# Performance work log

Hardware: AMD Instinct MI355X
Metric: run time of the kernel (lower is better)

## Reference

```python
import jax, jax.numpy as jnp
import numpy as np

B, NUM_SLOTS, D, TOP_K = 2048, 128, 1024, 8
DH = D // 2  # route_mlp hidden


def setup_inputs() -> dict:
    key = jax.random.key(0)
    ks = jax.random.split(key, 16)
    s = 0.02
    return {
        "x": jax.random.normal(ks[0], (B, D), jnp.float32),
        "S": jax.random.normal(ks[1], (B, NUM_SLOTS, D), jnp.float32),
        # route_mlp: Linear(2D, D//2) -> GELU -> Linear(D//2, NUM_SLOTS)
        "w1": jax.random.normal(ks[2], (DH, 2 * D), jnp.float32) * s,
        "b1": jnp.zeros((DH,), jnp.float32),
        "w2": jax.random.normal(ks[3], (NUM_SLOTS, DH), jnp.float32) * s,
        "b2": jnp.zeros((NUM_SLOTS,), jnp.float32),
        # GRUCell(D, D): torch layout, gates ordered (r, z, n)
        "gru_wih": jax.random.normal(ks[4], (3 * D, D), jnp.float32) * s,
        "gru_whh": jax.random.normal(ks[5], (3 * D, D), jnp.float32) * s,
        "gru_bih": jnp.zeros((3 * D,), jnp.float32),
        "gru_bhh": jnp.zeros((3 * D,), jnp.float32),
        "wval": jax.random.normal(ks[6], (D, D), jnp.float32) * s,
        "bval": jnp.zeros((D,), jnp.float32),
        "wout": jax.random.normal(ks[7], (D, D), jnp.float32) * s,
        "bout": jnp.zeros((D,), jnp.float32),
        "tau": jnp.ones((1,), jnp.float32),
    }


def reference(x, S, w1, b1, w2, b2, gru_wih, gru_whh, gru_bih, gru_bhh,
              wval, bval, wout, bout, tau):
    # Routing: context = [x, mean over slots]
    slot_mean = S.mean(axis=1)                                  # [B, D]
    ctx = jnp.concatenate([x, slot_mean], axis=-1)              # [B, 2D]
    h = jax.nn.gelu(ctx @ w1.T + b1, approximate=False)         # [B, DH]
    route_logits = (h @ w2.T + b2) / (jnp.abs(tau) + 0.1)       # [B, NUM_SLOTS]

    topk_vals, topk_idx = jax.lax.top_k(route_logits, TOP_K)    # [B, K]
    topk_w = jax.nn.softmax(topk_vals, axis=-1)                 # [B, K]

    # Gather selected slot states
    slot_states = jnp.take_along_axis(S, topk_idx[:, :, None], axis=1)  # [B, K, D]

    # GRUCell (torch semantics). Input part shared across the K slots.
    gi = x @ gru_wih.T + gru_bih                                # [B, 3D]
    gh = slot_states @ gru_whh.T + gru_bhh                      # [B, K, 3D]
    gi_r, gi_z, gi_n = jnp.split(gi, 3, axis=-1)
    gh_r, gh_z, gh_n = jnp.split(gh, 3, axis=-1)
    r = jax.nn.sigmoid(gi_r[:, None, :] + gh_r)
    z = jax.nn.sigmoid(gi_z[:, None, :] + gh_z)
    n = jnp.tanh(gi_n[:, None, :] + r * gh_n)
    updated = (1.0 - z) * n + z * slot_states                   # [B, K, D]

    # Scatter updated states back into slot memory
    S_new = S.at[jnp.arange(B)[:, None], topk_idx].set(updated)

    # Weighted value readout
    values = updated @ wval.T + bval                            # [B, K, D]
    mixed = jnp.einsum('bkd,bk->bd', values, topk_w)            # [B, D]
    output = mixed @ wout.T + bout                              # [B, D]
    return output, S_new
```

## Files before the change

### kernel.cpp

```cpp
#include <hip/hip_runtime.h>
#include <math.h>
#include <stdint.h>

#define B_   2048
#define NS_  128
#define D_   1024
#define K_   8
#define DH_  512
#define G3_  3072

typedef unsigned short u16;
typedef short bf16x8 __attribute__((ext_vector_type(8)));
typedef float f32x4 __attribute__((ext_vector_type(4)));

__device__ __forceinline__ float bf2f(u16 u) {
  union { unsigned i; float f; } v; v.i = ((unsigned)u) << 16; return v.f;
}
__device__ __forceinline__ u16 f2bf(float f) {
  unsigned x = __float_as_uint(f);
  return (u16)((x + 0x7fffu + ((x >> 16) & 1u)) >> 16);
}

#define AS1C(p) ((const __attribute__((address_space(1))) void*)(uintptr_t)(p))
#define AS3(p)  ((__attribute__((address_space(3))) void*)(unsigned)(uintptr_t)(p))

template<int DO_COPY>
__global__ __launch_bounds__(256)
void sp_copymean(const float* __restrict__ S, float* __restrict__ Snew,
                 float* __restrict__ mean) {
  const int b = blockIdx.x;
  const int t = threadIdx.x, d0 = t * 4;
  const f32x4* src = (const f32x4*)(S + (size_t)b * NS_ * D_) + t;
  f32x4* dst = (f32x4*)(Snew + (size_t)b * NS_ * D_) + t;
  double a0 = 0, a1 = 0, a2 = 0, a3 = 0;
  #pragma unroll 4
  for (int s = 0; s < NS_; ++s) {
    f32x4 v = __builtin_nontemporal_load(src);
    if (DO_COPY) __builtin_nontemporal_store(v, dst);
    a0 += v[0]; a1 += v[1]; a2 += v[2]; a3 += v[3];
    src += 256; dst += 256;
  }
  float4 m;
  m.x = (float)(a0 * (1.0 / 128.0)); m.y = (float)(a1 * (1.0 / 128.0));
  m.z = (float)(a2 * (1.0 / 128.0)); m.w = (float)(a3 * (1.0 / 128.0));
  *(float4*)&mean[(size_t)b * D_ + d0] = m;
}

__global__ __launch_bounds__(256)
void sp_prep(const float* __restrict__ x, const float* __restrict__ wih,
             const float* __restrict__ whh, const float* __restrict__ wout,
             const float* __restrict__ wval, const float* __restrict__ bval,
             const float* __restrict__ bout,
             u16* __restrict__ xb, u16* __restrict__ wihb,
             u16* __restrict__ whhb, u16* __restrict__ woutb,
             u16* __restrict__ wvalT, float* __restrict__ brow) {
  __shared__ u16 tile[64][65];
  const int blk = blockIdx.x;
  const int t = threadIdx.x;
  if (blk < 1024) {
    for (int i = blk * 256 + t; i < 2359296; i += 1024 * 256) {
      const float* s; u16* d; int off;
      if (i < 524288)       { s = x;    d = xb;    off = i; }
      else if (i < 1310720) { s = wih;  d = wihb;  off = i - 524288; }
      else if (i < 2097152) { s = whh;  d = whhb;  off = i - 1310720; }
      else                  { s = wout; d = woutb; off = i - 2097152; }
      float4 v = ((const float4*)s)[off];
      ushort4 o;
      o.x = f2bf(v.x); o.y = f2bf(v.y); o.z = f2bf(v.z); o.w = f2bf(v.w);
      ((ushort4*)d)[off] = o;
    }
  } else if (blk < 1280) {
    const int tb = blk - 1024;
    const int bx = tb & 15, by = tb >> 4;
    const int r = t >> 4, c4 = (t & 15) * 4;
    #pragma unroll
    for (int p = 0; p < 4; ++p) {
      const int row = by * 64 + p * 16 + r;
      float4 v = *(const float4*)&wval[(size_t)row * D_ + bx * 64 + c4];
      tile[p * 16 + r][c4 + 0] = f2bf(v.x);
      tile[p * 16 + r][c4 + 1] = f2bf(v.y);
      tile[p * 16 + r][c4 + 2] = f2bf(v.z);
      tile[p * 16 + r][c4 + 3] = f2bf(v.w);
    }
    __syncthreads();
    #pragma unroll
    for (int p = 0; p < 4; ++p) {
      const int jr = p * 16 + r;
      ushort4 o;
      o.x = tile[c4 + 0][jr];
      o.y = tile[c4 + 1][jr];
      o.z = tile[c4 + 2][jr];
      o.w = tile[c4 + 3][jr];
      *(ushort4*)&wvalT[(size_t)(bx * 64 + jr) * D_ + by * 64 + c4] = o;
    }
  } else {
    const int w = t >> 6, l = t & 63;
    const int i = (blk - 1280) * 4 + w;
    float s = 0.f;
    const float* wr = &wout[(size_t)i * D_ + l * 16];
    const float* bv = &bval[l * 16];
    #pragma unroll
    for (int j = 0; j < 16; j += 4) {
      float4 w4 = *(const float4*)&wr[j];
      float4 b4 = *(const float4*)&bv[j];
      s += w4.x * b4.x + w4.y * b4.y + w4.z * b4.z + w4.w * b4.w;
    }
    #pragma unroll
    for (int off = 32; off > 0; off >>= 1) s += __shfl_xor(s, off);
    if (l == 0) brow[i] = s + bout[i];
  }
}

__global__ __launch_bounds__(256)
void sp_gemm1(const float* __restrict__ x, const float* __restrict__ mean,
              const float* __restrict__ w1, const float* __restrict__ bias1,
              float* __restrict__ h) {
  __shared__ float As[16][68];
  __shared__ float Bs[16][36];
  int wg = blockIdx.x;
  wg = (wg & 7) * 64 + (wg >> 3);
  const int n0 = (wg & 15) * 32;
  const int m0 = (wg >> 4) * 64;
  const int t = threadIdx.x;
  const int tx = t & 15, ty = t >> 4;
  float acc[4][2] = {};
  const int sr = t >> 2, sc = (t & 3) * 4;
  for (int k0 = 0; k0 < 2 * D_; k0 += 16) {
    const float* src = (k0 < D_) ? (x + k0) : (mean + (k0 - D_));
    float4 va = *(const float4*)&src[(size_t)(m0 + sr) * D_ + sc];
    As[sc + 0][sr] = va.x; As[sc + 1][sr] = va.y; As[sc + 2][sr] = va.z; As[sc + 3][sr] = va.w;
    if (t < 128) {
      const int bn = t >> 2, bc = (t & 3) * 4;
      float4 vb = *(const float4*)&w1[(size_t)(n0 + bn) * (2 * D_) + k0 + bc];
      Bs[bc + 0][bn] = vb.x; Bs[bc + 1][bn] = vb.y; Bs[bc + 2][bn] = vb.z; Bs[bc + 3][bn] = vb.w;
    }
    __syncthreads();
    #pragma unroll
    for (int kk = 0; kk < 16; ++kk) {
      float4 a = *(const float4*)&As[kk][ty * 4];
      float2 bb = *(const float2*)&Bs[kk][tx * 2];
      acc[0][0] = fmaf(a.x, bb.x, acc[0][0]); acc[0][1] = fmaf(a.x, bb.y, acc[0][1]);
      acc[1][0] = fmaf(a.y, bb.x, acc[1][0]); acc[1][1] = fmaf(a.y, bb.y, acc[1][1]);
      acc[2][0] = fmaf(a.z, bb.x, acc[2][0]); acc[2][1] = fmaf(a.z, bb.y, acc[2][1]);
      acc[3][0] = fmaf(a.w, bb.x, acc[3][0]); acc[3][1] = fmaf(a.w, bb.y, acc[3][1]);
    }
    __syncthreads();
  }
  #pragma unroll
  for (int i = 0; i < 4; ++i) {
    #pragma unroll
    for (int j = 0; j < 2; ++j) {
      const int r = m0 + ty * 4 + i, c = n0 + tx * 2 + j;
      float v = acc[i][j] + bias1[c];
      v = 0.5f * v * (1.0f + erff(v * 0.70710678118654752f));
      h[(size_t)r * DH_ + c] = v;
    }
  }
}

__global__ __launch_bounds__(64)
void sp_route_topk(const float* __restrict__ h, const float* __restrict__ w2,
                   const float* __restrict__ b2, const float* __restrict__ tau,
                   const float* __restrict__ S,
                   int* __restrict__ tki, float* __restrict__ tkw,
                   u16* __restrict__ slotb) {
  __shared__ float hs[DH_];
  __shared__ int sTki[K_];
  const int b = blockIdx.x, l = threadIdx.x;
  *(float4*)&hs[l * 4] = *(const float4*)&h[(size_t)b * DH_ + l * 4];
  *(float4*)&hs[256 + l * 4] = *(const float4*)&h[(size_t)b * DH_ + 256 + l * 4];
  __syncthreads();
  const double invd = 1.0 / ((double)fabsf(tau[0]) + 0.1);
  float v[2]; int id[2];
  #pragma unroll
  for (int c = 0; c < 2; ++c) {
    const int n = c * 64 + l;
    const float* wr = &w2[(size_t)n * DH_];
    double s = 0.0;
    for (int j = 0; j < DH_; j += 4) {
      float4 w4 = *(const float4*)&wr[j];
      s += (double)hs[j] * (double)w4.x;
      s += (double)hs[j + 1] * (double)w4.y;
      s += (double)hs[j + 2] * (double)w4.z;
      s += (double)hs[j + 3] * (double)w4.w;
    }
    v[c] = (float)((s + (double)b2[n]) * invd);
    id[c] = n;
  }
  float m0f = 0.f, sum = 0.f, mye = 0.f; int myi = 0;
  for (int r = 0; r < 8; ++r) {
    float mv; int mi;
    if (v[1] > v[0]) { mv = v[1]; mi = id[1]; } else { mv = v[0]; mi = id[0]; }
    #pragma unroll
    for (int off = 32; off > 0; off >>= 1) {
      float ov = __shfl_xor(mv, off);
      int oi = __shfl_xor(mi, off);
      if (ov > mv || (ov == mv && oi < mi)) { mv = ov; mi = oi; }
    }
    if (r == 0) m0f = mv;
    float er = expf(mv - m0f);
    sum += er;
    if (l == r) { mye = er; myi = mi; }
    if (mi == id[0]) v[0] = -3.0e38f;
    if (mi == id[1]) v[1] = -3.0e38f;
  }
  if (l < 8) {
    tki[b * K_ + l] = myi; tkw[b * K_ + l] = mye / sum;
    sTki[l] = myi;
  }
  __syncthreads();
  #pragma unroll
  for (int k = 0; k < K_; ++k) {
    const int s = sTki[k];
    const float4* src = (const float4*)&S[((size_t)b * NS_ + s) * D_];
    ushort4* dst = (ushort4*)&slotb[((size_t)b * K_ + k) * D_];
    #pragma unroll
    for (int c = 0; c < 4; ++c) {
      float4 vv = src[c * 64 + l];
      ushort4 o;
      o.x = f2bf(vv.x); o.y = f2bf(vv.y); o.z = f2bf(vv.z); o.w = f2bf(vv.w);
      dst[c * 64 + l] = o;
    }
  }
}

template<int EPI>
__global__ __launch_bounds__(256)
void sp_gemm_bf16(const u16* __restrict__ A, const u16* __restrict__ Bm,
                  void* __restrict__ Cv, const float* __restrict__ bias,
                  int M, int N, int Kd, int nbx) {
  __shared__ u16 lA[128 * 32];
  __shared__ u16 lB[128 * 32];
  int wg = blockIdx.x;
  {
    const int nwg = nbx * ((M + 127) >> 7);
    const int cpx = nwg >> 3;
    wg = (wg & 7) * cpx + (wg >> 3);
  }
  const int m0 = (wg / nbx) * 128, n0 = (wg % nbx) * 128;
  const int t = threadIdx.x;
  const int lane = t & 63;
  const int w = t >> 6;
  const int wm = w >> 1, wn = w & 1;

  f32x4 acc[4][4] = {};

  const int srow = t >> 2;
  const int scol = (t & 3) * 8;
  const u16* gA0 = A + (size_t)(m0 + srow) * Kd + scol;
  const u16* gA1 = A + (size_t)(m0 + 64 + srow) * Kd + scol;
  const u16* gB0 = Bm + (size_t)(n0 + srow) * Kd + scol;
  const u16* gB1 = Bm + (size_t)(n0 + 64 + srow) * Kd + scol;
  u16* lAw = &lA[(t & 192) * 8];
  u16* lBw = &lB[(t & 192) * 8];

  const int kb = (lane >> 4) * 8;
  const int rA = wm * 64 + (lane & 15);
  const int rB = wn * 64 + (lane & 15);

  for (int k0 = 0; k0 < Kd; k0 += 32) {
    __builtin_amdgcn_global_load_lds(AS1C(gA0 + k0), AS3(lAw), 16, 0, 0);
    __builtin_amdgcn_global_load_lds(AS1C(gA1 + k0), AS3(lAw + 2048), 16, 0, 0);
    __builtin_amdgcn_global_load_lds(AS1C(gB0 + k0), AS3(lBw), 16, 0, 0);
    __builtin_amdgcn_global_load_lds(AS1C(gB1 + k0), AS3(lBw + 2048), 16, 0, 0);
    __syncthreads();
    bf16x8 af[4], bfr[4];
    #pragma unroll
    for (int fm = 0; fm < 4; ++fm)
      af[fm] = *(const bf16x8*)&lA[(rA + fm * 16) * 32 + kb];
    #pragma unroll
    for (int fn = 0; fn < 4; ++fn)
      bfr[fn] = *(const bf16x8*)&lB[(rB + fn * 16) * 32 + kb];
    #pragma unroll
    for (int fm = 0; fm < 4; ++fm) {
      #pragma unroll
      for (int fn = 0; fn < 4; ++fn)
        acc[fm][fn] = __builtin_amdgcn_mfma_f32_16x16x32_bf16(af[fm], bfr[fn], acc[fm][fn], 0, 0, 0);
    }
    __syncthreads();
  }

  #pragma unroll
  for (int fm = 0; fm < 4; ++fm) {
    #pragma unroll
    for (int fn = 0; fn < 4; ++fn) {
      #pragma unroll
      for (int i = 0; i < 4; ++i) {
        const int r = m0 + wm * 64 + fm * 16 + (lane >> 4) * 4 + i;
        const int c = n0 + wn * 64 + fn * 16 + (lane & 15);
        float v = acc[fm][fn][i];
        if constexpr (EPI >= 2) v += bias[c];
        if constexpr (EPI == 0 || EPI == 2)
          ((float*)Cv)[(size_t)r * N + c] = v;
        else
          ((u16*)Cv)[(size_t)r * N + c] = f2bf(v);
      }
    }
  }
}

template<bool DIRECT>
__global__ __launch_bounds__(256, 2)
void sp_gh_gru(const u16* __restrict__ slotb, const u16* __restrict__ whhb,
               const u16* __restrict__ gib, const float* __restrict__ bih,
               const float* __restrict__ bhh, const int* __restrict__ tki,
               const float* __restrict__ tkw, float* __restrict__ dst,
               u16* __restrict__ umixb) {
  __shared__ u16 lA[128 * 32];
  __shared__ u16 lB[192 * 32];
  __shared__ int   sTki[128];
  __shared__ float sTkw[128];
  int wg = blockIdx.x;
  wg = (wg & 7) * 256 + (wg >> 3);
  const int mt = wg >> 4, db = wg & 15;
  const int m0 = mt * 128, d0 = db * 64;
  const int t = threadIdx.x;
  const int lane = t & 63, w = t >> 6;
  const int wm = w >> 1, wn = w & 1;
  const int lane15 = lane & 15, hi = lane >> 4;

  if (t < 128) { sTki[t] = tki[m0 + t]; sTkw[t] = tkw[m0 + t]; }

  f32x4 acc[4][6] = {};

  const int srow = t >> 2;
  const int scol = (t & 3) * 8;
  const u16* gA0 = slotb + (size_t)(m0 + srow) * D_ + scol;
  const u16* gA1 = slotb + (size_t)(m0 + 64 + srow) * D_ + scol;
  const u16* gB0 = whhb + (size_t)(d0 + srow) * D_ + scol;
  const u16* gB1 = whhb + (size_t)(D_ + d0 + srow) * D_ + scol;
  const u16* gB2 = whhb + (size_t)(2 * D_ + d0 + srow) * D_ + scol;
  u16* lAw = &lA[(t & 192) * 8];
  u16* lBw = &lB[(t & 192) * 8];

  const int kb = hi * 8;
  const int rA = wm * 64 + lane15;
  const int rB = wn * 32 + lane15;

  for (int k0 = 0; k0 < D_; k0 += 32) {
    __builtin_amdgcn_global_load_lds(AS1C(gA0 + k0), AS3(lAw), 16, 0, 0);
    __builtin_amdgcn_global_load_lds(AS1C(gA1 + k0), AS3(lAw + 2048), 16, 0, 0);
    __builtin_amdgcn_global_load_lds(AS1C(gB0 + k0), AS3(lBw), 16, 0, 0);
    __builtin_amdgcn_global_load_lds(AS1C(gB1 + k0), AS3(lBw + 2048), 16, 0, 0);
    __builtin_amdgcn_global_load_lds(AS1C(gB2 + k0), AS3(lBw + 4096), 16, 0, 0);
    __syncthreads();
    bf16x8 af[4], bfr[6];
    #pragma unroll
    for (int fm = 0; fm < 4; ++fm)
      af[fm] = *(const bf16x8*)&lA[(rA + fm * 16) * 32 + kb];
    #pragma unroll
    for (int g = 0; g < 3; ++g) {
      #pragma unroll
      for (int f = 0; f < 2; ++f)
        bfr[g * 2 + f] = *(const bf16x8*)&lB[(g * 64 + rB + f * 16) * 32 + kb];
    }
    #pragma unroll
    for (int fm = 0; fm < 4; ++fm) {
      #pragma unroll
      for (int fn = 0; fn < 6; ++fn)
        acc[fm][fn] = __builtin_amdgcn_mfma_f32_16x16x32_bf16(af[fm], bfr[fn], acc[fm][fn], 0, 0, 0);
    }
    __syncthreads();
  }

  #pragma unroll
  for (int fm = 0; fm < 4; ++fm) {
    const int rbase = wm * 64 + fm * 16 + hi * 4;
    const int bglob = (m0 + rbase) >> 3;
    #pragma unroll
    for (int f = 0; f < 2; ++f) {
      const int dg = d0 + wn * 32 + f * 16 + lane15;
      const float Gr = bf2f(gib[(size_t)bglob * G3_ + dg])          + bih[dg];
      const float Gz = bf2f(gib[(size_t)bglob * G3_ + D_ + dg])     + bih[D_ + dg];
      const float Gn = bf2f(gib[(size_t)bglob * G3_ + 2 * D_ + dg]) + bih[2 * D_ + dg];
      const float Br = bhh[dg], Bz = bhh[D_ + dg], Bn = bhh[2 * D_ + dg];
      float part = 0.f;
      #pragma unroll
      for (int i = 0; i < 4; ++i) {
        const int row = rbase + i;
        const int grow = m0 + row;
        const float slot = bf2f(slotb[(size_t)grow * D_ + dg]);
        const float rr = acc[fm][f][i] + Br;
        const float zz = acc[fm][f + 2][i] + Bz;
        const float nn = acc[fm][f + 4][i] + Bn;
        const float rg = 1.f / (1.f + expf(-(Gr + rr)));
        const float zg = 1.f / (1.f + expf(-(Gz + zz)));
        const float ng = tanhf(Gn + rg * nn);
        const float uv = (1.f - zg) * ng + zg * slot;
        part = fmaf(sTkw[row], uv, part);
        if (DIRECT)
          dst[((size_t)bglob * NS_ + sTki[row]) * D_ + dg] = uv;
        else
          dst[(size_t)grow * D_ + dg] = uv;
      }
      part += __shfl_xor(part, 16);
      if ((hi & 1) == 0)
        umixb[(size_t)bglob * D_ + dg] = f2bf(part);
    }
  }
}

__global__ __launch_bounds__(256)
void sp_copy_scatter(const float* __restrict__ S, const float* __restrict__ upd,
                     const int* __restrict__ tki, float* __restrict__ Snew) {
  const int b = blockIdx.x, t = threadIdx.x;
  const int d0 = t * 4;
  int idx[K_];
  #pragma unroll
  for (int k = 0; k < K_; ++k) idx[k] = tki[b * K_ + k];
  for (int s = 0; s < NS_; ++s) {
    int sk = -1;
    #pragma unroll
    for (int k = 0; k < K_; ++k) if (idx[k] == s) sk = k;
    float4 v;
    if (sk >= 0) v = *(const float4*)&upd[((size_t)b * K_ + sk) * D_ + d0];
    else         v = *(const float4*)&S[((size_t)b * NS_ + s) * D_ + d0];
    *(float4*)&Snew[((size_t)b * NS_ + s) * D_ + d0] = v;
  }
}

extern "C" void kernel_launch(void* const* d_in, const int* in_sizes, int n_in,
                              void* d_out, int out_size, void* d_ws, size_t ws_size,
                              hipStream_t stream) {
  const float* x    = (const float*)d_in[0];
  const float* S    = (const float*)d_in[1];
  const float* w1   = (const float*)d_in[2];
  const float* b1   = (const float*)d_in[3];
  const float* w2   = (const float*)d_in[4];
  const float* b2   = (const float*)d_in[5];
  const float* wih  = (const float*)d_in[6];
  const float* whh  = (const float*)d_in[7];
  const float* bih  = (const float*)d_in[8];
  const float* bhh  = (const float*)d_in[9];
  const float* wval = (const float*)d_in[10];
  const float* bval = (const float*)d_in[11];
  const float* wout = (const float*)d_in[12];
  const float* bout = (const float*)d_in[13];
  const float* tau  = (const float*)d_in[14];

  float* out  = (float*)d_out;
  float* Snew = out + (size_t)B_ * D_;

  const bool bigws = ws_size >= (size_t)400 * 1024 * 1024;
  char* bigbase = bigws ? (char*)d_ws : (char*)Snew;
  size_t bo = 0;
  auto balloc = [&](size_t bytes) -> void* {
    void* p = bigbase + bo; bo += (bytes + 255) & ~(size_t)255; return p;
  };

  float* mean  = (float*)balloc((size_t)B_ * D_ * 4);
  float* h     = (float*)balloc((size_t)B_ * DH_ * 4);
  u16* xb      = (u16*)balloc((size_t)B_ * D_ * 2);
  u16* wihb    = (u16*)balloc((size_t)G3_ * D_ * 2);
  u16* whhb    = (u16*)balloc((size_t)G3_ * D_ * 2);
  u16* woutb   = (u16*)balloc((size_t)D_ * D_ * 2);
  u16* wvalTb  = (u16*)balloc((size_t)D_ * D_ * 2);
  u16* Wrob    = (u16*)balloc((size_t)D_ * D_ * 2);
  u16* gib     = (u16*)balloc((size_t)B_ * G3_ * 2);
  u16* slotb   = (u16*)balloc((size_t)B_ * K_ * D_ * 2);
  u16* umixb   = (u16*)balloc((size_t)B_ * D_ * 2);
  float* brow  = (float*)balloc((size_t)D_ * 4);

  char* wsb = (char*)d_ws;
  size_t so = bigws ? bo : 0;
  auto salloc = [&](size_t bytes) -> void* {
    void* p = wsb + so; so += (bytes + 255) & ~(size_t)255; return p;
  };
  int*   tki = (int*)salloc((size_t)B_ * K_ * 4);
  float* tkw = (float*)salloc((size_t)B_ * K_ * 4);
  float* upd = bigws ? nullptr : (float*)salloc((size_t)B_ * K_ * D_ * 4);

  if (bigws) sp_copymean<1><<<B_, 256, 0, stream>>>(S, Snew, mean);
  else       sp_copymean<0><<<B_, 256, 0, stream>>>(S, Snew, mean);

  sp_prep<<<1536, 256, 0, stream>>>(x, wih, whh, wout, wval, bval, bout,
                                    xb, wihb, whhb, woutb, wvalTb, brow);

  sp_gemm_bf16<1><<<64, 256, 0, stream>>>(woutb, wvalTb, Wrob, nullptr, D_, D_, D_, 8);

  sp_gemm1<<<512, 256, 0, stream>>>(x, mean, w1, b1, h);

  sp_route_topk<<<B_, 64, 0, stream>>>(h, w2, b2, tau, S, tki, tkw, slotb);

  sp_gemm_bf16<1><<<384, 256, 0, stream>>>(xb, wihb, gib, nullptr, B_, G3_, D_, G3_ / 128);

  if (bigws)
    sp_gh_gru<true><<<2048, 256, 0, stream>>>(slotb, whhb, gib, bih, bhh,
                                              tki, tkw, Snew, umixb);
  else
    sp_gh_gru<false><<<2048, 256, 0, stream>>>(slotb, whhb, gib, bih, bhh,
                                               tki, tkw, upd, umixb);

  sp_gemm_bf16<2><<<128, 256, 0, stream>>>(umixb, Wrob, out, brow, B_, D_, D_, 8);

  if (!bigws)
    sp_copy_scatter<<<B_, 256, 0, stream>>>(S, upd, tki, Snew);
}
```

Before: 827.3 us.

## Merge copy/mean with weight prep and fuse independent GEMMs into one launch

The S copy/mean kernel and the weight-conversion prep kernel become one launch with block-range dispatch. The x@Wih GEMM, the routing GEMM1 (retiled to 64x64 per block) and the Wout·WvalT GEMM also become one launch, so independent work runs side by side. The gi GEMM moves ahead of top-k routing. This removes launch gaps and tail underutilisation, but larger LDS per block in the merged kernel may lower occupancy for the fp32 GEMM path.

```diff
diff --git a/kernel.cpp b/kernel.cpp
--- a/kernel.cpp
+++ b/kernel.cpp
@@ -26,39 +26,38 @@
 
 template<int DO_COPY>
 __global__ __launch_bounds__(256)
-void sp_copymean(const float* __restrict__ S, float* __restrict__ Snew,
-                 float* __restrict__ mean) {
-  const int b = blockIdx.x;
-  const int t = threadIdx.x, d0 = t * 4;
-  const f32x4* src = (const f32x4*)(S + (size_t)b * NS_ * D_) + t;
-  f32x4* dst = (f32x4*)(Snew + (size_t)b * NS_ * D_) + t;
-  double a0 = 0, a1 = 0, a2 = 0, a3 = 0;
-  #pragma unroll 4
-  for (int s = 0; s < NS_; ++s) {
-    f32x4 v = __builtin_nontemporal_load(src);
-    if (DO_COPY) __builtin_nontemporal_store(v, dst);
-    a0 += v[0]; a1 += v[1]; a2 += v[2]; a3 += v[3];
-    src += 256; dst += 256;
-  }
-  float4 m;
-  m.x = (float)(a0 * (1.0 / 128.0)); m.y = (float)(a1 * (1.0 / 128.0));
-  m.z = (float)(a2 * (1.0 / 128.0)); m.w = (float)(a3 * (1.0 / 128.0));
-  *(float4*)&mean[(size_t)b * D_ + d0] = m;
-}
-
-__global__ __launch_bounds__(256)
-void sp_prep(const float* __restrict__ x, const float* __restrict__ wih,
-             const float* __restrict__ whh, const float* __restrict__ wout,
-             const float* __restrict__ wval, const float* __restrict__ bval,
-             const float* __restrict__ bout,
-             u16* __restrict__ xb, u16* __restrict__ wihb,
-             u16* __restrict__ whhb, u16* __restrict__ woutb,
-             u16* __restrict__ wvalT, float* __restrict__ brow) {
+void sp_copyprep(const float* __restrict__ S, float* __restrict__ Snew,
+                 float* __restrict__ mean,
+                 const float* __restrict__ x, const float* __restrict__ wih,
+                 const float* __restrict__ whh, const float* __restrict__ wout,
+                 const float* __restrict__ wval, const float* __restrict__ bval,
+                 const float* __restrict__ bout,
+                 u16* __restrict__ xb, u16* __restrict__ wihb,
+                 u16* __restrict__ whhb, u16* __restrict__ woutb,
+                 u16* __restrict__ wvalT, float* __restrict__ brow) {
   __shared__ u16 tile[64][65];
   const int blk = blockIdx.x;
   const int t = threadIdx.x;
-  if (blk < 1024) {
-    for (int i = blk * 256 + t; i < 2359296; i += 1024 * 256) {
+  if (blk < 2048) {
+    const int b = blk;
+    const int d0 = t * 4;
+    const f32x4* src = (const f32x4*)(S + (size_t)b * NS_ * D_) + t;
+    f32x4* dst = (f32x4*)(Snew + (size_t)b * NS_ * D_) + t;
+    double a0 = 0, a1 = 0, a2 = 0, a3 = 0;
+    #pragma unroll 4
+    for (int s = 0; s < NS_; ++s) {
+      f32x4 v = __builtin_nontemporal_load(src);
+      if (DO_COPY) __builtin_nontemporal_store(v, dst);
+      a0 += v[0]; a1 += v[1]; a2 += v[2]; a3 += v[3];
+      src += 256; dst += 256;
+    }
+    float4 m;
+    m.x = (float)(a0 * (1.0 / 128.0)); m.y = (float)(a1 * (1.0 / 128.0));
+    m.z = (float)(a2 * (1.0 / 128.0)); m.w = (float)(a3 * (1.0 / 128.0));
+    *(float4*)&mean[(size_t)b * D_ + d0] = m;
+  } else if (blk < 3072) {
+    const int cid = blk - 2048;
+    for (int i = cid * 256 + t; i < 2359296; i += 1024 * 256) {
       const float* s; u16* d; int off;
       if (i < 524288)       { s = x;    d = xb;    off = i; }
       else if (i < 1310720) { s = wih;  d = wihb;  off = i - 524288; }
@@ -69,8 +68,8 @@
       o.x = f2bf(v.x); o.y = f2bf(v.y); o.z = f2bf(v.z); o.w = f2bf(v.w);
       ((ushort4*)d)[off] = o;
     }
-  } else if (blk < 1280) {
-    const int tb = blk - 1024;
+  } else if (blk < 3328) {
+    const int tb = blk - 3072;
     const int bx = tb & 15, by = tb >> 4;
     const int r = t >> 4, c4 = (t & 15) * 4;
     #pragma unroll
@@ -95,7 +94,7 @@
     }
   } else {
     const int w = t >> 6, l = t & 63;
-    const int i = (blk - 1280) * 4 + w;
+    const int i = (blk - 3328) * 4 + w;
     float s = 0.f;
     const float* wr = &wout[(size_t)i * D_ + l * 16];
     const float* bv = &bval[l * 16];
@@ -111,50 +110,136 @@
   }
 }
 
+template<int EPI>
+__device__ __forceinline__ void gemm_bf16_body(
+    const u16* __restrict__ A, const u16* __restrict__ Bm,
+    void* __restrict__ Cv, const float* __restrict__ bias,
+    int M, int N, int Kd, int nbx, int wg, u16* lA, u16* lB) {
+  {
+    const int nwg = nbx * ((M + 127) >> 7);
+    const int cpx = nwg >> 3;
+    wg = (wg & 7) * cpx + (wg >> 3);
+  }
+  const int m0 = (wg / nbx) * 128, n0 = (wg % nbx) * 128;
+  const int t = threadIdx.x;
+  const int lane = t & 63;
+  const int w = t >> 6;
+  const int wm = w >> 1, wn = w & 1;
+
+  f32x4 acc[4][4] = {};
+
+  const int srow = t >> 2;
+  const int scol = (t & 3) * 8;
+  const u16* gA0 = A + (size_t)(m0 + srow) * Kd + scol;
+  const u16* gA1 = A + (size_t)(m0 + 64 + srow) * Kd + scol;
+  const u16* gB0 = Bm + (size_t)(n0 + srow) * Kd + scol;
+  const u16* gB1 = Bm + (size_t)(n0 + 64 + srow) * Kd + scol;
+  u16* lAw = lA + (t & 192) * 8;
+  u16* lBw = lB + (t & 192) * 8;
+
+  const int kb = (lane >> 4) * 8;
+  const int rA = wm * 64 + (lane & 15);
+  const int rB = wn * 64 + (lane & 15);
+
+  for (int k0 = 0; k0 < Kd; k0 += 32) {
+    __builtin_amdgcn_global_load_lds(AS1C(gA0 + k0), AS3(lAw), 16, 0, 0);
+    __builtin_amdgcn_global_load_lds(AS1C(gA1 + k0), AS3(lAw + 2048), 16, 0, 0);
+    __builtin_amdgcn_global_load_lds(AS1C(gB0 + k0), AS3(lBw), 16, 0, 0);
+    __builtin_amdgcn_global_load_lds(AS1C(gB1 + k0), AS3(lBw + 2048), 16, 0, 0);
+    __syncthreads();
+    bf16x8 af[4], bfr[4];
+    #pragma unroll
+    for (int fm = 0; fm < 4; ++fm)
+      af[fm] = *(const bf16x8*)&lA[(rA + fm * 16) * 32 + kb];
+    #pragma unroll
+    for (int fn = 0; fn < 4; ++fn)
+      bfr[fn] = *(const bf16x8*)&lB[(rB + fn * 16) * 32 + kb];
+    #pragma unroll
+    for (int fm = 0; fm < 4; ++fm) {
+      #pragma unroll
+      for (int fn = 0; fn < 4; ++fn)
+        acc[fm][fn] = __builtin_amdgcn_mfma_f32_16x16x32_bf16(af[fm], bfr[fn], acc[fm][fn], 0, 0, 0);
+    }
+    __syncthreads();
+  }
+
+  #pragma unroll
+  for (int fm = 0; fm < 4; ++fm) {
+    #pragma unroll
+    for (int fn = 0; fn < 4; ++fn) {
+      #pragma unroll
+      for (int i = 0; i < 4; ++i) {
+        const int r = m0 + wm * 64 + fm * 16 + (lane >> 4) * 4 + i;
+        const int c = n0 + wn * 64 + fn * 16 + (lane & 15);
+        float v = acc[fm][fn][i];
+        if constexpr (EPI == 2) {
+          ((float*)Cv)[(size_t)r * N + c] = v + bias[c];
+        } else {
+          ((u16*)Cv)[(size_t)r * N + c] = f2bf(v);
+        }
+      }
+    }
+  }
+}
+
 __global__ __launch_bounds__(256)
-void sp_gemm1(const float* __restrict__ x, const float* __restrict__ mean,
-              const float* __restrict__ w1, const float* __restrict__ bias1,
-              float* __restrict__ h) {
-  __shared__ float As[16][68];
-  __shared__ float Bs[16][36];
-  int wg = blockIdx.x;
-  wg = (wg & 7) * 64 + (wg >> 3);
-  const int n0 = (wg & 15) * 32;
-  const int m0 = (wg >> 4) * 64;
+void sp_mid(const u16* __restrict__ xb, const u16* __restrict__ wihb,
+            u16* __restrict__ gib,
+            const float* __restrict__ x, const float* __restrict__ mean,
+            const float* __restrict__ w1, const float* __restrict__ b1,
+            float* __restrict__ h,
+            const u16* __restrict__ woutb, const u16* __restrict__ wvalTb,
+            u16* __restrict__ Wrob) {
+  __shared__ u16 lA[128 * 32];
+  __shared__ u16 lB[128 * 32];
+  const int blk = blockIdx.x;
   const int t = threadIdx.x;
-  const int tx = t & 15, ty = t >> 4;
-  float acc[4][2] = {};
-  const int sr = t >> 2, sc = (t & 3) * 4;
-  for (int k0 = 0; k0 < 2 * D_; k0 += 16) {
-    const float* src = (k0 < D_) ? (x + k0) : (mean + (k0 - D_));
-    float4 va = *(const float4*)&src[(size_t)(m0 + sr) * D_ + sc];
-    As[sc + 0][sr] = va.x; As[sc + 1][sr] = va.y; As[sc + 2][sr] = va.z; As[sc + 3][sr] = va.w;
-    if (t < 128) {
-      const int bn = t >> 2, bc = (t & 3) * 4;
-      float4 vb = *(const float4*)&w1[(size_t)(n0 + bn) * (2 * D_) + k0 + bc];
-      Bs[bc + 0][bn] = vb.x; Bs[bc + 1][bn] = vb.y; Bs[bc + 2][bn] = vb.z; Bs[bc + 3][bn] = vb.w;
-    }
-    __syncthreads();
-    #pragma unroll
-    for (int kk = 0; kk < 16; ++kk) {
-      float4 a = *(const float4*)&As[kk][ty * 4];
-      float2 bb = *(const float2*)&Bs[kk][tx * 2];
-      acc[0][0] = fmaf(a.x, bb.x, acc[0][0]); acc[0][1] = fmaf(a.x, bb.y, acc[0][1]);
-      acc[1][0] = fmaf(a.y, bb.x, acc[1][0]); acc[1][1] = fmaf(a.y, bb.y, acc[1][1]);
-      acc[2][0] = fmaf(a.z, bb.x, acc[2][0]); acc[2][1] = fmaf(a.z, bb.y, acc[2][1]);
-      acc[3][0] = fmaf(a.w, bb.x, acc[3][0]); acc[3][1] = fmaf(a.w, bb.y, acc[3][1]);
-    }
-    __syncthreads();
-  }
-  #pragma unroll
-  for (int i = 0; i < 4; ++i) {
-    #pragma unroll
-    for (int j = 0; j < 2; ++j) {
-      const int r = m0 + ty * 4 + i, c = n0 + tx * 2 + j;
-      float v = acc[i][j] + bias1[c];
-      v = 0.5f * v * (1.0f + erff(v * 0.70710678118654752f));
-      h[(size_t)r * DH_ + c] = v;
-    }
+  if (blk < 384) {
+    gemm_bf16_body<1>(xb, wihb, gib, nullptr, B_, G3_, D_, G3_ / 128, blk, lA, lB);
+  } else if (blk < 640) {
+    float (*As)[68] = (float(*)[68])lA;
+    float (*Bs)[68] = (float(*)[68])lB;
+    int wg = blk - 384;
+    wg = (wg & 7) * 32 + (wg >> 3);
+    const int m0 = (wg >> 3) * 64;
+    const int n0 = (wg & 7) * 64;
+    const int tx = t & 15, ty = t >> 4;
+    float acc[4][4] = {};
+    const int sr = t >> 2, sc = (t & 3) * 4;
+    for (int k0 = 0; k0 < 2 * D_; k0 += 16) {
+      const float* src = (k0 < D_) ? (x + k0) : (mean + (k0 - D_));
+      float4 va = *(const float4*)&src[(size_t)(m0 + sr) * D_ + sc];
+      As[sc + 0][sr] = va.x; As[sc + 1][sr] = va.y; As[sc + 2][sr] = va.z; As[sc + 3][sr] = va.w;
+      float4 vb = *(const float4*)&w1[(size_t)(n0 + sr) * (2 * D_) + k0 + sc];
+      Bs[sc + 0][sr] = vb.x; Bs[sc + 1][sr] = vb.y; Bs[sc + 2][sr] = vb.z; Bs[sc + 3][sr] = vb.w;
+      __syncthreads();
+      #pragma unroll
+      for (int kk = 0; kk < 16; ++kk) {
+        float4 a4 = *(const float4*)&As[kk][ty * 4];
+        float4 b4 = *(const float4*)&Bs[kk][tx * 4];
+        acc[0][0] = fmaf(a4.x, b4.x, acc[0][0]); acc[0][1] = fmaf(a4.x, b4.y, acc[0][1]);
+        acc[0][2] = fmaf(a4.x, b4.z, acc[0][2]); acc[0][3] = fmaf(a4.x, b4.w, acc[0][3]);
+        acc[1][0] = fmaf(a4.y, b4.x, acc[1][0]); acc[1][1] = fmaf(a4.y, b4.y, acc[1][1]);
+        acc[1][2] = fmaf(a4.y, b4.z, acc[1][2]); acc[1][3] = fmaf(a4.y, b4.w, acc[1][3]);
+        acc[2][0] = fmaf(a4.z, b4.x, acc[2][0]); acc[2][1] = fmaf(a4.z, b4.y, acc[2][1]);
+        acc[2][2] = fmaf(a4.z, b4.z, acc[2][2]); acc[2][3] = fmaf(a4.z, b4.w, acc[2][3]);
+        acc[3][0] = fmaf(a4.w, b4.x, acc[3][0]); acc[3][1] = fmaf(a4.w, b4.y, acc[3][1]);
+        acc[3][2] = fmaf(a4.w, b4.z, acc[3][2]); acc[3][3] = fmaf(a4.w, b4.w, acc[3][3]);
+      }
+      __syncthreads();
+    }
+    #pragma unroll
+    for (int i = 0; i < 4; ++i) {
+      #pragma unroll
+      for (int j = 0; j < 4; ++j) {
+        const int r = m0 + ty * 4 + i, c = n0 + tx * 4 + j;
+        float v = acc[i][j] + b1[c];
+        v = 0.5f * v * (1.0f + erff(v * 0.70710678118654752f));
+        h[(size_t)r * DH_ + c] = v;
+      }
+    }
+  } else {
+    gemm_bf16_body<1>(woutb, wvalTb, Wrob, nullptr, D_, D_, D_, 8, blk - 640, lA, lB);
   }
 }
 
@@ -231,72 +316,7 @@
                   int M, int N, int Kd, int nbx) {
   __shared__ u16 lA[128 * 32];
   __shared__ u16 lB[128 * 32];
-  int wg = blockIdx.x;
-  {
-    const int nwg = nbx * ((M + 127) >> 7);
-    const int cpx = nwg >> 3;
-    wg = (wg & 7) * cpx + (wg >> 3);
-  }
-  const int m0 = (wg / nbx) * 128, n0 = (wg % nbx) * 128;
-  const int t = threadIdx.x;
-  const int lane = t & 63;
-  const int w = t >> 6;
-  const int wm = w >> 1, wn = w & 1;
-
-  f32x4 acc[4][4] = {};
-
-  const int srow = t >> 2;
-  const int scol = (t & 3) * 8;
-  const u16* gA0 = A + (size_t)(m0 + srow) * Kd + scol;
-  const u16* gA1 = A + (size_t)(m0 + 64 + srow) * Kd + scol;
-  const u16* gB0 = Bm + (size_t)(n0 + srow) * Kd + scol;
-  const u16* gB1 = Bm + (size_t)(n0 + 64 + srow) * Kd + scol;
-  u16* lAw = &lA[(t & 192) * 8];
-  u16* lBw = &lB[(t & 192) * 8];
-
-  const int kb = (lane >> 4) * 8;
-  const int rA = wm * 64 + (lane & 15);
-  const int rB = wn * 64 + (lane & 15);
-
-  for (int k0 = 0; k0 < Kd; k0 += 32) {
-    __builtin_amdgcn_global_load_lds(AS1C(gA0 + k0), AS3(lAw), 16, 0, 0);
-    __builtin_amdgcn_global_load_lds(AS1C(gA1 + k0), AS3(lAw + 2048), 16, 0, 0);
-    __builtin_amdgcn_global_load_lds(AS1C(gB0 + k0), AS3(lBw), 16, 0, 0);
-    __builtin_amdgcn_global_load_lds(AS1C(gB1 + k0), AS3(lBw + 2048), 16, 0, 0);
-    __syncthreads();
-    bf16x8 af[4], bfr[4];
-    #pragma unroll
-    for (int fm = 0; fm < 4; ++fm)
-      af[fm] = *(const bf16x8*)&lA[(rA + fm * 16) * 32 + kb];
-    #pragma unroll
-    for (int fn = 0; fn < 4; ++fn)
-      bfr[fn] = *(const bf16x8*)&lB[(rB + fn * 16) * 32 + kb];
-    #pragma unroll
-    for (int fm = 0; fm < 4; ++fm) {
-      #pragma unroll
-      for (int fn = 0; fn < 4; ++fn)
-        acc[fm][fn] = __builtin_amdgcn_mfma_f32_16x16x32_bf16(af[fm], bfr[fn], acc[fm][fn], 0, 0, 0);
-    }
-    __syncthreads();
-  }
-
-  #pragma unroll
-  for (int fm = 0; fm < 4; ++fm) {
-    #pragma unroll
-    for (int fn = 0; fn < 4; ++fn) {
-      #pragma unroll
-      for (int i = 0; i < 4; ++i) {
-        const int r = m0 + wm * 64 + fm * 16 + (lane >> 4) * 4 + i;
-        const int c = n0 + wn * 64 + fn * 16 + (lane & 15);
-        float v = acc[fm][fn][i];
-        if constexpr (EPI >= 2) v += bias[c];
-        if constexpr (EPI == 0 || EPI == 2)
-          ((float*)Cv)[(size_t)r * N + c] = v;
-        else
-          ((u16*)Cv)[(size_t)r * N + c] = f2bf(v);
-      }
-    }
-  }
+  gemm_bf16_body<EPI>(A, Bm, Cv, bias, M, N, Kd, nbx, blockIdx.x, lA, lB);
 }
 
 template<bool DIRECT>
@@ -470,19 +490,19 @@
   float* tkw = (float*)salloc((size_t)B_ * K_ * 4);
   float* upd = bigws ? nullptr : (float*)salloc((size_t)B_ * K_ * D_ * 4);
 
-  if (bigws) sp_copymean<1><<<B_, 256, 0, stream>>>(S, Snew, mean);
-  else       sp_copymean<0><<<B_, 256, 0, stream>>>(S, Snew, mean);
-
-  sp_prep<<<1536, 256, 0, stream>>>(x, wih, whh, wout, wval, bval, bout,
-                                    xb, wihb, whhb, woutb, wvalTb, brow);
-
-  sp_gemm_bf16<1><<<64, 256, 0, stream>>>(woutb, wvalTb, Wrob, nullptr, D_, D_, D_, 8);
-
-  sp_gemm1<<<512, 256, 0, stream>>>(x, mean, w1, b1, h);
+  if (bigws)
+    sp_copyprep<1><<<3584, 256, 0, stream>>>(S, Snew, mean, x, wih, whh, wout,
+                                             wval, bval, bout, xb, wihb, whhb,
+                                             woutb, wvalTb, brow);
+  else
+    sp_copyprep<0><<<3584, 256, 0, stream>>>(S, Snew, mean, x, wih, whh, wout,
+                                             wval, bval, bout, xb, wihb, whhb,
+                                             woutb, wvalTb, brow);
+
+  sp_mid<<<704, 256, 0, stream>>>(xb, wihb, gib, x, mean, w1, b1, h,
+                                  woutb, wvalTb, Wrob);
 
   sp_route_topk<<<B_, 64, 0, stream>>>(h, w2, b2, tau, S, tki, tkw, slotb);
-
-  sp_gemm_bf16<1><<<384, 256, 0, stream>>>(xb, wihb, gib, nullptr, B_, G3_, D_, G3_ / 128);
 
   if (bigws)
     sp_gh_gru<true><<<2048, 256, 0, stream>>>(slotb, whhb, gib, bih, bhh,
```

Result: faster. 782.5 us (-5.4%).
